# Performance work log

Measured on AMD Instinct MI355X. Metric: run time of the kernel, lower is better.

The kernel has to match this reference:

```python
import jax, jax.numpy as jnp
import numpy as np

QDEPTH = 8
WIDTH = 64
HEIGHT = 64
WIRES = 12  # ceil(log2(64*64))
BATCH = 1024


def setup_inputs() -> dict:
    key = jax.random.key(0)
    k1, k2 = jax.random.split(key)
    x = jax.random.normal(k1, (BATCH, 1, WIDTH, HEIGHT), dtype=jnp.float32)
    # torch.nn.Parameter(torch.randn(weight_shape) * 0.4)
    weights = jax.random.normal(k2, (QDEPTH, WIRES, 3), dtype=jnp.float32) * 0.4
    return {"x": x, "weights": weights, "reps": 1}


def _rot_matrices(angles):
    # angles: (L, W, 3) -> (L, W, 2, 2) complex64; Rot(phi, theta, omega) = RZ(omega) RY(theta) RZ(phi)
    phi, theta, omega = angles[..., 0], angles[..., 1], angles[..., 2]
    c = jnp.cos(theta * 0.5).astype(jnp.complex64)
    s = jnp.sin(theta * 0.5).astype(jnp.complex64)
    ep = jnp.exp(-0.5j * (phi + omega).astype(jnp.complex64))  # e^{-i(phi+omega)/2}
    em = jnp.exp(-0.5j * (phi - omega).astype(jnp.complex64))  # e^{-i(phi-omega)/2}
    row0 = jnp.stack([ep * c, -jnp.conj(em) * s], axis=-1)
    row1 = jnp.stack([em * s, jnp.conj(ep) * c], axis=-1)
    return jnp.stack([row0, row1], axis=-2)


def _apply_1q(state, U, wire):
    # state: (B, 2, 2, ..., 2); apply 2x2 U on axis wire+1
    ax = wire + 1
    s = jnp.moveaxis(state, ax, -1)
    s = s @ U.T  # out[..., i] = sum_j U[i, j] s[..., j]
    return jnp.moveaxis(s, -1, ax)


def _apply_cnot(state, control, target):
    c, t = control + 1, target + 1
    s0, s1 = jnp.split(state, 2, axis=c)   # control = 0 / 1 halves
    s1 = jnp.flip(s1, axis=t)              # X on target where control = 1
    return jnp.concatenate([s0, s1], axis=c)


def _sel_layer(state, mats_l, r):
    # one StronglyEntanglingLayers layer: Rot on every wire, then CNOT ring of range r
    for w in range(WIRES):
        state = _apply_1q(state, mats_l[w], w)
    for w in range(WIRES):
        state = _apply_cnot(state, w, (w + r) % WIRES)
    return state


def _circuit(state, weights, reps):
    mats = _rot_matrices(jnp.tanh(weights))  # qw_map.tanh applied to raw weights
    for _ in range(reps):
        for l in range(QDEPTH):
            r = (l % (WIRES - 1)) + 1  # PennyLane default ranges
            layer = jax.checkpoint(lambda s, m, _r=r: _sel_layer(s, m, _r))
            state = layer(state, mats[l])
    return state


def reference(x, weights, reps):
    b = x.shape[0]
    v = x.reshape(b, -1)  # (b, 4096)
    norm = jnp.linalg.norm(v, axis=-1, keepdims=True)
    v = (v / norm).astype(jnp.complex64)
    state = v.reshape((b,) + (2,) * WIRES)
    state = _circuit(state, weights, reps)
    out = state.reshape(b, -1) * norm
    return out.reshape(b, 1, WIDTH, HEIGHT)
```

## Files before the change

### kernel.cpp

```cpp
#include <hip/hip_runtime.h>

#define WIRES   12
#define NSTATE  4096
#define QDEPTH  8
#define BLOCK   256
#define PER_T   16

using f2 = __attribute__((ext_vector_type(2))) float;

__device__ __forceinline__ int slotf(int a) { return a + (a >> 4); }

constexpr int colF(int l, int j) {
    int rr = (l % (WIRES - 1)) + 1;
    int v = 1 << j;
    for (int k = WIRES - 1; k >= 0; --k) {
        int bc = 11 - k;
        int bt = 11 - ((k + rr) % WIRES);
        v ^= ((v >> bc) & 1) << bt;
    }
    return v;
}
struct ColsT { int v[QDEPTH][WIRES]; };
constexpr ColsT mkCols() {
    ColsT c{};
    for (int l = 0; l < QDEPTH; ++l)
        for (int j = 0; j < WIRES; ++j) c.v[l][j] = colF(l, j);
    return c;
}
static __device__ const ColsT COLS = mkCols();

__global__ void mats_kernel(const float* __restrict__ wts, f2* __restrict__ mg)
{
    int t = blockIdx.x * blockDim.x + threadIdx.x;
    if (t >= QDEPTH * WIRES) return;
    float phi   = tanhf(wts[t * 3 + 0]);
    float theta = tanhf(wts[t * 3 + 1]);
    float omega = tanhf(wts[t * 3 + 2]);
    float c  = cosf(theta * 0.5f);
    float s  = sinf(theta * 0.5f);
    float a  = 0.5f * (phi + omega);
    float bm = 0.5f * (phi - omega);
    float ca = cosf(a),  sa = sinf(a);
    float cb = cosf(bm), sb = sinf(bm);
    f2* m = mg + t * 8;
    m[0] = f2{ c * ca,  c * ca};
    m[1] = f2{ c * sa, -c * sa};
    m[2] = f2{-s * cb, -s * cb};
    m[3] = f2{ s * sb, -s * sb};
    m[4] = f2{ s * cb,  s * cb};
    m[5] = f2{ s * sb, -s * sb};
    m[6] = f2{ c * ca,  c * ca};
    m[7] = f2{-c * sa,  c * sa};
}

template<int P>
__device__ __forceinline__ void gate(f2 r[PER_T], const f2* __restrict__ m)
{
    const f2 u00r = m[0], u00w = m[1], u01r = m[2], u01w = m[3];
    const f2 u10r = m[4], u10w = m[5], u11r = m[6], u11w = m[7];
    #pragma unroll
    for (int pr = 0; pr < PER_T / 2; pr += 2) {
        const int k0 = ((pr >> P) << (P + 1)) | (pr & ((1 << P) - 1));
        const int k1 = k0 | (1 << P);
        const int q  = pr + 1;
        const int j0 = ((q >> P) << (P + 1)) | (q & ((1 << P) - 1));
        const int j1 = j0 | (1 << P);
        f2 a0, b0, a1, b1;
        asm("v_pk_mul_f32 %0, %4, %8\n\t"
            "v_pk_mul_f32 %1, %4, %12\n\t"
            "v_pk_mul_f32 %2, %6, %8\n\t"
            "v_pk_mul_f32 %3, %6, %12\n\t"
            "v_pk_fma_f32 %0, %4, %9, %0 op_sel:[1,0,0] op_sel_hi:[0,1,1]\n\t"
            "v_pk_fma_f32 %1, %4, %13, %1 op_sel:[1,0,0] op_sel_hi:[0,1,1]\n\t"
            "v_pk_fma_f32 %2, %6, %9, %2 op_sel:[1,0,0] op_sel_hi:[0,1,1]\n\t"
            "v_pk_fma_f32 %3, %6, %13, %3 op_sel:[1,0,0] op_sel_hi:[0,1,1]\n\t"
            "v_pk_fma_f32 %0, %5, %10, %0\n\t"
            "v_pk_fma_f32 %1, %5, %14, %1\n\t"
            "v_pk_fma_f32 %2, %7, %10, %2\n\t"
            "v_pk_fma_f32 %3, %7, %14, %3\n\t"
            "v_pk_fma_f32 %0, %5, %11, %0 op_sel:[1,0,0] op_sel_hi:[0,1,1]\n\t"
            "v_pk_fma_f32 %1, %5, %15, %1 op_sel:[1,0,0] op_sel_hi:[0,1,1]\n\t"
            "v_pk_fma_f32 %2, %7, %11, %2 op_sel:[1,0,0] op_sel_hi:[0,1,1]\n\t"
            "v_pk_fma_f32 %3, %7, %15, %3 op_sel:[1,0,0] op_sel_hi:[0,1,1]"
            : "=&v"(a0), "=&v"(b0), "=&v"(a1), "=&v"(b1)
            : "v"(r[k0]), "v"(r[k1]), "v"(r[j0]), "v"(r[j1]),
              "v"(u00r), "v"(u00w), "v"(u01r), "v"(u01w),
              "v"(u10r), "v"(u10w), "v"(u11r), "v"(u11w));
        r[k0] = a0; r[k1] = b0; r[j0] = a1; r[j1] = b1;
    }
}

__global__ __launch_bounds__(BLOCK, 4) void qsim_kernel(
    const float* __restrict__ x,
    const f2*    __restrict__ mats_g,
    const int*   __restrict__ reps_ptr,
    float*       __restrict__ out,
    int write_mode)
{
    __shared__ f2 st[4352];

    const int g   = threadIdx.x;
    const int b   = blockIdx.x;
    const int ghi = g >> 4, glo = g & 15;
    const int w1b = 17 * g;
    const int rb1 = 272 * ghi + glo;
    const int rb2 = 17 * ghi + glo;

    const float4* xb4 = (const float4*)(x + (size_t)b * NSTATE) + g * 4;
    f2 r[PER_T];
    #pragma unroll
    for (int c = 0; c < 4; ++c) {
        float4 v = xb4[c];
        r[4*c+0] = f2{v.x, 0.f};
        r[4*c+1] = f2{v.y, 0.f};
        r[4*c+2] = f2{v.z, 0.f};
        r[4*c+3] = f2{v.w, 0.f};
    }

    const int reps = reps_ptr[0];
    for (int rep = 0; rep < reps; ++rep) {
        #pragma unroll 1
        for (int l = 0; l < QDEPTH; ++l) {
            const f2* M = mats_g + l * WIRES * 8;

            gate<3>(r, M + 8*8);  gate<2>(r, M + 9*8);
            gate<1>(r, M + 10*8); gate<0>(r, M + 11*8);

            #pragma unroll
            for (int k = 0; k < PER_T; ++k) st[w1b + k] = r[k];
            __syncthreads();
            #pragma unroll
            for (int k = 0; k < PER_T; ++k) r[k] = st[rb1 + 17 * k];

            gate<3>(r, M + 4*8); gate<2>(r, M + 5*8);
            gate<1>(r, M + 6*8); gate<0>(r, M + 7*8);

            #pragma unroll
            for (int k = 0; k < PER_T; ++k) st[rb1 + 17 * k] = r[k];
            __syncthreads();
            #pragma unroll
            for (int k = 0; k < PER_T; ++k) r[k] = st[rb2 + 272 * k];

            gate<3>(r, M + 0*8); gate<2>(r, M + 1*8);
            gate<1>(r, M + 2*8); gate<0>(r, M + 3*8);

            #pragma unroll
            for (int k = 0; k < PER_T; ++k) st[rb2 + 272 * k] = r[k];
            __syncthreads();

            int Fg = 0;
            #pragma unroll
            for (int j = 0; j < 8; ++j)
                Fg ^= ((g >> j) & 1) ? COLS.v[l][4 + j] : 0;
            const int c0 = COLS.v[l][0], c1 = COLS.v[l][1];
            const int c2 = COLS.v[l][2], c3 = COLS.v[l][3];
            #pragma unroll
            for (int k = 0; k < PER_T; ++k) {
                int ck = ((k & 1) ? c0 : 0) ^ ((k & 2) ? c1 : 0) ^
                         ((k & 4) ? c2 : 0) ^ ((k & 8) ? c3 : 0);
                r[k] = st[slotf(Fg ^ ck)];
            }
            __syncthreads();
        }
    }

    if (write_mode == 0) {
        float4* ob4 = (float4*)(out + (size_t)b * NSTATE) + g * 4;
        #pragma unroll
        for (int c = 0; c < 4; ++c)
            ob4[c] = make_float4(r[4*c].x, r[4*c+1].x, r[4*c+2].x, r[4*c+3].x);
    } else {
        float4* ob4 = (float4*)((float2*)out + (size_t)b * NSTATE) + g * 8;
        #pragma unroll
        for (int k = 0; k < PER_T; k += 2)
            ob4[k >> 1] = make_float4(r[k].x, r[k].y, r[k+1].x, r[k+1].y);
    }
}

extern "C" void kernel_launch(void* const* d_in, const int* in_sizes, int n_in,
                              void* d_out, int out_size, void* d_ws, size_t ws_size,
                              hipStream_t stream) {
    const float* x    = (const float*)d_in[0];
    const float* wts  = (const float*)d_in[1];
    const int*   reps = (const int*)d_in[2];
    float*       out  = (float*)d_out;
    f2*          mg   = (f2*)d_ws;
    (void)in_sizes; (void)n_in; (void)ws_size;

    const int write_mode = (out_size >= 2 * 1024 * NSTATE) ? 1 : 0;

    mats_kernel<<<1, 128, 0, stream>>>(wts, mg);
    qsim_kernel<<<1024, BLOCK, 0, stream>>>(x, mg, reps, out, write_mode);
}
```

Before: 145.6 us.

## Factor Rot gates into diagonal phases plus real RY rotations

Each Rot gate is split as RZ·RY·RZ. The RZ phases of all wires in a layer are combined into two diagonal phase multiplies per layer, one at the start and one at the end, built from per-thread and per-register phase tables. The remaining RY gates are real 2x2 rotations and need 8 packed ops instead of 16. This cuts the FLOPs in the gate application but adds sincos work and extra diagonal multiplies per layer.

Result: faster. 134.9 us (-7.4%).

```diff
diff --git a/kernel.cpp b/kernel.cpp
--- a/kernel.cpp
+++ b/kernel.cpp
@@ -29,35 +29,48 @@
 }
 static __device__ const ColsT COLS = mkCols();
 
-__global__ void mats_kernel(const float* __restrict__ wts, f2* __restrict__ mg)
-{
-    int t = blockIdx.x * blockDim.x + threadIdx.x;
-    if (t >= QDEPTH * WIRES) return;
-    float phi   = tanhf(wts[t * 3 + 0]);
-    float theta = tanhf(wts[t * 3 + 1]);
-    float omega = tanhf(wts[t * 3 + 2]);
-    float c  = cosf(theta * 0.5f);
-    float s  = sinf(theta * 0.5f);
-    float a  = 0.5f * (phi + omega);
-    float bm = 0.5f * (phi - omega);
-    float ca = cosf(a),  sa = sinf(a);
-    float cb = cosf(bm), sb = sinf(bm);
-    f2* m = mg + t * 8;
-    m[0] = f2{ c * ca,  c * ca};
-    m[1] = f2{ c * sa, -c * sa};
-    m[2] = f2{-s * cb, -s * cb};
-    m[3] = f2{ s * sb, -s * sb};
-    m[4] = f2{ s * cb,  s * cb};
-    m[5] = f2{ s * sb, -s * sb};
-    m[6] = f2{ c * ca,  c * ca};
-    m[7] = f2{-c * sa,  c * sa};
+#define OFF_KP 288
+#define OFF_KW 544
+#define OFF_AN 800
+
+__global__ void setup_kernel(const float* __restrict__ wts, f2* __restrict__ mg)
+{
+    const int t = threadIdx.x;
+    if (t < QDEPTH * WIRES) {
+        float th = tanhf(wts[t * 3 + 1]);
+        float c = cosf(0.5f * th), s = sinf(0.5f * th);
+        mg[(t / 12) * 36 + (t % 12) * 3 + 0] = f2{ c,  c};
+        mg[(t / 12) * 36 + (t % 12) * 3 + 1] = f2{-s, -s};
+        mg[(t / 12) * 36 + (t % 12) * 3 + 2] = f2{ s,  s};
+    }
+    if (t < 64) {
+        int l = t >> 3, j = t & 7;
+        float aP = 0.5f * tanhf(wts[(l * 12 + (7  - j)) * 3 + 0]);
+        float aW = 0.5f * tanhf(wts[(l * 12 + (11 - j)) * 3 + 2]);
+        mg[OFF_AN + l * 8 + j] = f2{aP, aW};
+    }
+    {
+        int l = t >> 5, k = (t >> 1) & 15;
+        bool isW = (t & 1) != 0;
+        float ph = 0.f;
+        #pragma unroll
+        for (int j = 0; j < 4; ++j) {
+            int wire  = isW ? (3 - j) : (11 - j);
+            int comp  = isW ? 2 : 0;
+            float a   = 0.5f * tanhf(wts[(l * 12 + wire) * 3 + comp]);
+            ph += ((k >> j) & 1) ? a : -a;
+        }
+        float s, c;
+        sincosf(ph, &s, &c);
+        int base = isW ? OFF_KW : OFF_KP;
+        mg[base + l * 32 + k * 2 + 0] = f2{ c, c};
+        mg[base + l * 32 + k * 2 + 1] = f2{-s, s};
+    }
 }
 
 template<int P>
-__device__ __forceinline__ void gate(f2 r[PER_T], const f2* __restrict__ m)
-{
-    const f2 u00r = m[0], u00w = m[1], u01r = m[2], u01w = m[3];
-    const f2 u10r = m[4], u10w = m[5], u11r = m[6], u11w = m[7];
+__device__ __forceinline__ void gateR(f2 r[PER_T], f2 cc, f2 ms, f2 ss)
+{
     #pragma unroll
     for (int pr = 0; pr < PER_T / 2; pr += 2) {
         const int k0 = ((pr >> P) << (P + 1)) | (pr & ((1 << P) - 1));
@@ -67,32 +80,56 @@
         const int j1 = j0 | (1 << P);
         f2 a0, b0, a1, b1;
         asm("v_pk_mul_f32 %0, %4, %8\n\t"
-            "v_pk_mul_f32 %1, %4, %12\n\t"
+            "v_pk_mul_f32 %1, %4, %10\n\t"
             "v_pk_mul_f32 %2, %6, %8\n\t"
-            "v_pk_mul_f32 %3, %6, %12\n\t"
-            "v_pk_fma_f32 %0, %4, %9, %0 op_sel:[1,0,0] op_sel_hi:[0,1,1]\n\t"
-            "v_pk_fma_f32 %1, %4, %13, %1 op_sel:[1,0,0] op_sel_hi:[0,1,1]\n\t"
-            "v_pk_fma_f32 %2, %6, %9, %2 op_sel:[1,0,0] op_sel_hi:[0,1,1]\n\t"
-            "v_pk_fma_f32 %3, %6, %13, %3 op_sel:[1,0,0] op_sel_hi:[0,1,1]\n\t"
-            "v_pk_fma_f32 %0, %5, %10, %0\n\t"
-            "v_pk_fma_f32 %1, %5, %14, %1\n\t"
-            "v_pk_fma_f32 %2, %7, %10, %2\n\t"
-            "v_pk_fma_f32 %3, %7, %14, %3\n\t"
-            "v_pk_fma_f32 %0, %5, %11, %0 op_sel:[1,0,0] op_sel_hi:[0,1,1]\n\t"
-            "v_pk_fma_f32 %1, %5, %15, %1 op_sel:[1,0,0] op_sel_hi:[0,1,1]\n\t"
-            "v_pk_fma_f32 %2, %7, %11, %2 op_sel:[1,0,0] op_sel_hi:[0,1,1]\n\t"
-            "v_pk_fma_f32 %3, %7, %15, %3 op_sel:[1,0,0] op_sel_hi:[0,1,1]"
+            "v_pk_mul_f32 %3, %6, %10\n\t"
+            "v_pk_fma_f32 %0, %5, %9, %0\n\t"
+            "v_pk_fma_f32 %1, %5, %8, %1\n\t"
+            "v_pk_fma_f32 %2, %7, %9, %2\n\t"
+            "v_pk_fma_f32 %3, %7, %8, %3"
             : "=&v"(a0), "=&v"(b0), "=&v"(a1), "=&v"(b1)
             : "v"(r[k0]), "v"(r[k1]), "v"(r[j0]), "v"(r[j1]),
-              "v"(u00r), "v"(u00w), "v"(u01r), "v"(u01w),
-              "v"(u10r), "v"(u10w), "v"(u11r), "v"(u11w));
+              "v"(cc), "v"(ms), "v"(ss));
         r[k0] = a0; r[k1] = b0; r[j0] = a1; r[j1] = b1;
     }
+}
+
+__device__ __forceinline__ void dmul2(f2& a0, f2& a1, f2 d0r, f2 d0w,
+                                      f2 d1r, f2 d1w)
+{
+    f2 o0, o1;
+    asm("v_pk_mul_f32 %0, %2, %4\n\t"
+        "v_pk_mul_f32 %1, %3, %6\n\t"
+        "v_pk_fma_f32 %0, %2, %5, %0 op_sel:[1,0,0] op_sel_hi:[0,1,1]\n\t"
+        "v_pk_fma_f32 %1, %3, %7, %1 op_sel:[1,0,0] op_sel_hi:[0,1,1]"
+        : "=&v"(o0), "=&v"(o1)
+        : "v"(a0), "v"(a1), "v"(d0r), "v"(d0w), "v"(d1r), "v"(d1w));
+    a0 = o0; a1 = o1;
+}
+
+__device__ __forceinline__ void diag(f2 r[PER_T], const f2* __restrict__ AN,
+                                     const f2* __restrict__ KF, int g, bool isW)
+{
+    float ph = 0.f;
+    #pragma unroll
+    for (int j = 0; j < 8; ++j) {
+        float a = isW ? AN[j].y : AN[j].x;
+        ph += ((g >> j) & 1) ? a : -a;
+    }
+    float s, c;
+    sincosf(ph, &s, &c);
+    const f2 Lr = f2{c, c}, Lw = f2{-s, s};
+    #pragma unroll
+    for (int k = 0; k < PER_T; k += 2)
+        dmul2(r[k], r[k + 1], Lr, Lw, Lr, Lw);
+    #pragma unroll
+    for (int k = 0; k < PER_T; k += 2)
+        dmul2(r[k], r[k + 1], KF[2*k], KF[2*k + 1], KF[2*k + 2], KF[2*k + 3]);
 }
 
 __global__ __launch_bounds__(BLOCK, 4) void qsim_kernel(
     const float* __restrict__ x,
-    const f2*    __restrict__ mats_g,
+    const f2*    __restrict__ mg,
     const int*   __restrict__ reps_ptr,
     float*       __restrict__ out,
     int write_mode)
@@ -121,10 +158,17 @@
     for (int rep = 0; rep < reps; ++rep) {
         #pragma unroll 1
         for (int l = 0; l < QDEPTH; ++l) {
-            const f2* M = mats_g + l * WIRES * 8;
-
-            gate<3>(r, M + 8*8);  gate<2>(r, M + 9*8);
-            gate<1>(r, M + 10*8); gate<0>(r, M + 11*8);
+            const f2* CS = mg + l * 36;
+            const f2* KP = mg + OFF_KP + l * 32;
+            const f2* KW = mg + OFF_KW + l * 32;
+            const f2* AN = mg + OFF_AN + l * 8;
+
+            diag(r, AN, KP, g, false);
+
+            gateR<3>(r, CS[8*3],  CS[8*3+1],  CS[8*3+2]);
+            gateR<2>(r, CS[9*3],  CS[9*3+1],  CS[9*3+2]);
+            gateR<1>(r, CS[10*3], CS[10*3+1], CS[10*3+2]);
+            gateR<0>(r, CS[11*3], CS[11*3+1], CS[11*3+2]);
 
             #pragma unroll
             for (int k = 0; k < PER_T; ++k) st[w1b + k] = r[k];
@@ -132,8 +176,10 @@
             #pragma unroll
             for (int k = 0; k < PER_T; ++k) r[k] = st[rb1 + 17 * k];
 
-            gate<3>(r, M + 4*8); gate<2>(r, M + 5*8);
-            gate<1>(r, M + 6*8); gate<0>(r, M + 7*8);
+            gateR<3>(r, CS[4*3], CS[4*3+1], CS[4*3+2]);
+            gateR<2>(r, CS[5*3], CS[5*3+1], CS[5*3+2]);
+            gateR<1>(r, CS[6*3], CS[6*3+1], CS[6*3+2]);
+            gateR<0>(r, CS[7*3], CS[7*3+1], CS[7*3+2]);
 
             #pragma unroll
             for (int k = 0; k < PER_T; ++k) st[rb1 + 17 * k] = r[k];
@@ -141,24 +187,30 @@
             #pragma unroll
             for (int k = 0; k < PER_T; ++k) r[k] = st[rb2 + 272 * k];
 
-            gate<3>(r, M + 0*8); gate<2>(r, M + 1*8);
-            gate<1>(r, M + 2*8); gate<0>(r, M + 3*8);
+            gateR<3>(r, CS[0*3], CS[0*3+1], CS[0*3+2]);
+            gateR<2>(r, CS[1*3], CS[1*3+1], CS[1*3+2]);
+            gateR<1>(r, CS[2*3], CS[2*3+1], CS[2*3+2]);
+            gateR<0>(r, CS[3*3], CS[3*3+1], CS[3*3+2]);
+
+            diag(r, AN, KW, g, true);
 
             #pragma unroll
             for (int k = 0; k < PER_T; ++k) st[rb2 + 272 * k] = r[k];
             __syncthreads();
 
-            int Fg = 0;
-            #pragma unroll
-            for (int j = 0; j < 8; ++j)
-                Fg ^= ((g >> j) & 1) ? COLS.v[l][4 + j] : 0;
-            const int c0 = COLS.v[l][0], c1 = COLS.v[l][1];
-            const int c2 = COLS.v[l][2], c3 = COLS.v[l][3];
-            #pragma unroll
-            for (int k = 0; k < PER_T; ++k) {
-                int ck = ((k & 1) ? c0 : 0) ^ ((k & 2) ? c1 : 0) ^
-                         ((k & 4) ? c2 : 0) ^ ((k & 8) ? c3 : 0);
-                r[k] = st[slotf(Fg ^ ck)];
+            {
+                int Fg = 0;
+                #pragma unroll
+                for (int j = 0; j < 8; ++j)
+                    Fg ^= ((g >> j) & 1) ? COLS.v[l][4 + j] : 0;
+                const int c0 = COLS.v[l][0], c1 = COLS.v[l][1];
+                const int c2 = COLS.v[l][2], c3 = COLS.v[l][3];
+                #pragma unroll
+                for (int k = 0; k < PER_T; ++k) {
+                    int ck = ((k & 1) ? c0 : 0) ^ ((k & 2) ? c1 : 0) ^
+                             ((k & 4) ? c2 : 0) ^ ((k & 8) ? c3 : 0);
+                    r[k] = st[slotf(Fg ^ ck)];
+                }
             }
             __syncthreads();
         }
@@ -189,6 +241,6 @@
 
     const int write_mode = (out_size >= 2 * 1024 * NSTATE) ? 1 : 0;
 
-    mats_kernel<<<1, 128, 0, stream>>>(wts, mg);
+    setup_kernel<<<1, 256, 0, stream>>>(wts, mg);
     qsim_kernel<<<1024, BLOCK, 0, stream>>>(x, mg, reps, out, write_mode);
 }
```
